# Performance work log

Measured on AMD Instinct MI355X. Metric: run time of the kernel, lower is better.

## Reference

```python
import jax, jax.numpy as jnp
import numpy as np

B, NQ, C = 2, 10000, 256
M, L, K = 8, 3, 4
D = C // M
LEVEL_SHAPES = [(100, 100), (50, 50), (25, 25)]


def setup_inputs() -> dict:
    key = jax.random.key(0)
    ks = jax.random.split(key, 16)
    inp = {
        "query": jax.random.normal(ks[0], (B, NQ, C), jnp.float32),
        "reference_points": jax.random.uniform(ks[1], (B, NQ, 2), jnp.float32),
        "value0": jax.random.normal(ks[2], (B, C) + LEVEL_SHAPES[0], jnp.float32),
        "value1": jax.random.normal(ks[3], (B, C) + LEVEL_SHAPES[1], jnp.float32),
        "value2": jax.random.normal(ks[4], (B, C) + LEVEL_SHAPES[2], jnp.float32),
        "Wv": jax.random.normal(ks[5], (C, C), jnp.float32) * 0.02,
        "bv": jnp.zeros((C,), jnp.float32),
        "Ws": jax.random.normal(ks[6], (M * L * K * 2, C), jnp.float32) * 0.05,
        "bs": jax.random.normal(ks[7], (M * L * K * 2,), jnp.float32),
        "Wa": jax.random.normal(ks[8], (M * L * K, C), jnp.float32) * 0.02,
        "ba": jnp.zeros((M * L * K,), jnp.float32),
        "Wo": jax.random.normal(ks[9], (C, C), jnp.float32) * 0.02,
        "bo": jnp.zeros((C,), jnp.float32),
    }
    return inp


def _bilinear_sample(vflat, px, py, H, W):
    """grid_sample bilinear, align_corners=False, padding_mode='zeros'.
    vflat: (B, M, H*W, D); px, py: (B, M, Q, K) pixel coords. -> (B, M, Q, K, D)
    """
    b, m, q, k = px.shape
    x0 = jnp.floor(px)
    y0 = jnp.floor(py)
    wx1 = px - x0  # frac weights (grad 1 w.r.t. px, matching grid_sample)
    wy1 = py - y0
    wx0 = 1.0 - wx1
    wy0 = 1.0 - wy1

    def gather(xi, yi):
        valid = ((xi >= 0) & (xi <= W - 1) & (yi >= 0) & (yi <= H - 1)).astype(vflat.dtype)
        xc = jnp.clip(xi, 0, W - 1).astype(jnp.int32)
        yc = jnp.clip(yi, 0, H - 1).astype(jnp.int32)
        idx = (yc * W + xc).reshape(b, m, q * k)
        g = jnp.take_along_axis(vflat, idx[..., None], axis=2)  # (B,M,QK,D)
        return g.reshape(b, m, q, k, -1) * valid[..., None]

    out = (gather(x0, y0) * (wx0 * wy0)[..., None]
           + gather(x0 + 1, y0) * (wx1 * wy0)[..., None]
           + gather(x0, y0 + 1) * (wx0 * wy1)[..., None]
           + gather(x0 + 1, y0 + 1) * (wx1 * wy1)[..., None])
    return out


def reference(query, reference_points, value0, value1, value2,
              Wv, bv, Ws, bs, Wa, ba, Wo, bo):
    bsz, nq, c = query.shape
    dt = query.dtype
    # sampling offsets and attention weights
    off = (query @ Ws.T + bs).reshape(bsz, nq, M, L, K, 2)
    attn = jax.nn.softmax((query @ Wa.T + ba).reshape(bsz, nq, M, L * K), axis=-1)
    attn = attn.reshape(bsz, nq, M, L, K)

    out = jnp.zeros((bsz, nq, M, D), dt)
    for li, v in enumerate([value0, value1, value2]):
        H, W = v.shape[2], v.shape[3]
        # conv1x1 value projection -> per-head maps (B, M, H*W, D)
        proj = jnp.einsum('bchw,oc->bohw', v, Wv) + bv[None, :, None, None]
        vflat = proj.reshape(bsz, M, D, H * W).transpose(0, 1, 3, 2)
        norm = jnp.asarray([W, H], dt)
        loc = reference_points[:, :, None, None, :] + off[:, :, :, li, :, :] / norm  # (B,Q,M,K,2)
        # grid = loc*2-1; pixel = (grid+1)*size/2 - 0.5 = loc*size - 0.5
        px = (loc[..., 0] * W - 0.5).transpose(0, 2, 1, 3)  # (B,M,Q,K)
        py = (loc[..., 1] * H - 0.5).transpose(0, 2, 1, 3)
        sampled = _bilinear_sample(vflat, px, py, H, W)  # (B,M,Q,K,D)
        out = out + jnp.einsum('bmqkd,bqmk->bqmd', sampled, attn[:, :, :, li, :])

    out = out.reshape(bsz, nq, c)
    return out @ Wo.T + bo
```

## Files before the change

### kernel.cpp

```cpp
#include <hip/hip_runtime.h>
#include <cstddef>

#define B_ 2
#define NQ_ 10000
#define C_ 256
#define M_ 8
#define L_ 3
#define K_ 4
#define D_ 32
#define P_ 13125

typedef unsigned short u16;
typedef __attribute__((ext_vector_type(8))) short short8;
typedef __attribute__((ext_vector_type(4))) float f32x4;

static __device__ __forceinline__ u16 f2bf(float f) {
    union { float f; unsigned u; } x; x.f = f;
    unsigned r = x.u + 0x7fffu + ((x.u >> 16) & 1u);
    return (u16)(r >> 16);
}
static __device__ __forceinline__ short8 cvt8(const float4& a, const float4& b) {
    short8 r;
    r[0] = (short)f2bf(a.x); r[1] = (short)f2bf(a.y);
    r[2] = (short)f2bf(a.z); r[3] = (short)f2bf(a.w);
    r[4] = (short)f2bf(b.x); r[5] = (short)f2bf(b.y);
    r[6] = (short)f2bf(b.z); r[7] = (short)f2bf(b.w);
    return r;
}

__global__ __launch_bounds__(256) void cvt_f32_bf16(
    const float* __restrict__ in, u16* __restrict__ out, int n8)
{
    const int i = blockIdx.x * 256 + threadIdx.x;
    if (i >= n8) return;
    const float4 a = *reinterpret_cast<const float4*>(in + (size_t)i * 8);
    const float4 b = *reinterpret_cast<const float4*>(in + (size_t)i * 8 + 4);
    *reinterpret_cast<short8*>(out + (size_t)i * 8) = cvt8(a, b);
}

__global__ __launch_bounds__(256) void cvt_weights(
    const float* __restrict__ Wv, const float* __restrict__ Ws,
    const float* __restrict__ Wa, const float* __restrict__ Wo,
    u16* __restrict__ wb)
{
    const int i = blockIdx.x * 256 + threadIdx.x;
    if (i >= 25600) return;
    const int g = i * 8;
    const float* src;
    if (g < 65536)       src = Wv + g;
    else if (g < 114688) src = Ws + (g - 65536);
    else if (g < 139264) src = Wa + (g - 114688);
    else                 src = Wo + (g - 139264);
    const float4 a = *reinterpret_cast<const float4*>(src);
    const float4 b = *reinterpret_cast<const float4*>(src + 4);
    *reinterpret_cast<short8*>(wb + g) = cvt8(a, b);
}

__global__ __launch_bounds__(256) void transpose_value(
    const float* __restrict__ v0, const float* __restrict__ v1,
    const float* __restrict__ v2, u16* __restrict__ Vt)
{
    constexpr int HWs[3]  = {10000, 2500, 625};
    constexpr int offs[3] = {0, 10000, 12500};

    const int z   = blockIdx.z;
    const int b   = z / 3;
    const int lvl = z % 3;
    const int HW  = HWs[lvl];
    const int p0  = blockIdx.x * 64;
    if (p0 >= HW) return;
    const int c0  = blockIdx.y * 64;

    const float* V = (lvl == 0 ? v0 : (lvl == 1 ? v1 : v2)) + (size_t)b * 256 * HW;

    __shared__ u16 tile[64][66];
    const int t  = threadIdx.x;
    const int pl = t & 63;
    const int cb = t >> 6;

    #pragma unroll
    for (int i = 0; i < 16; ++i) {
        int c = cb + i * 4;
        float vv = 0.f;
        if (p0 + pl < HW)
            vv = V[(size_t)(c0 + c) * HW + p0 + pl];
        tile[pl][c] = f2bf(vv);
    }
    __syncthreads();

    const int cl = t & 63;
    const int pb = t >> 6;
    #pragma unroll
    for (int i = 0; i < 16; ++i) {
        int p = pb + i * 4;
        if (p0 + p < HW)
            Vt[((size_t)b * P_ + offs[lvl] + p0 + p) * 256 + c0 + cl] = tile[p][cl];
    }
}

__global__ __launch_bounds__(512) void gemm_fused(
    const u16* __restrict__ Vt, const u16* __restrict__ qbf,
    const u16* __restrict__ Wvb, const float* __restrict__ bv,
    const u16* __restrict__ Wsb, const float* __restrict__ bs,
    const u16* __restrict__ Wab, const float* __restrict__ ba,
    u16* __restrict__ proj, float* __restrict__ S)
{
    __shared__ u16 Bs[64 * 264];

    const bool jobS = (blockIdx.x >= 416);
    const int  bid  = jobS ? (blockIdx.x - 416) : blockIdx.x;

    const int npanel    = jobS ? 5 : 4;
    const int nRowTiles = jobS ? 79 : 103;
    const int rows      = jobS ? (B_ * NQ_) : (B_ * P_);
    const int N1        = jobS ? 192 : 256;
    const int Ntot      = jobS ? 288 : 256;
    const u16* Aimg     = jobS ? qbf : Vt;
    const u16* B1b      = jobS ? Wsb : Wvb;
    const u16* B2b      = jobS ? Wab : Wvb;
    const float* bias1  = jobS ? bs : bv;
    const float* bias2  = jobS ? ba : bv;

    const int rlo  = bid & 7;
    const int tmp  = bid >> 3;
    const int panel = tmp % npanel;
    const int rowTile = (tmp / npanel) * 8 + rlo;
    if (rowTile >= nRowTiles) return;

    const int t  = threadIdx.x;
    const int w  = t >> 6;
    const int l  = t & 63;
    const int row0 = rowTile * 256 + w * 32;
    const int o0   = panel * 64;
    const int lr = l & 15;
    const int kb = (l >> 4) * 8;

    const int ra0 = min(row0 + lr,      rows - 1);
    const int ra1 = min(row0 + 16 + lr, rows - 1);
    const u16* Ap0 = Aimg + (size_t)ra0 * 256 + kb;
    const u16* Ap1 = Aimg + (size_t)ra1 * 256 + kb;

    short8 A0[4], A1[4];
    #pragma unroll
    for (int i = 0; i < 4; ++i) {
        A0[i] = *reinterpret_cast<const short8*>(Ap0 + i * 32);
        A1[i] = *reinterpret_cast<const short8*>(Ap1 + i * 32);
    }

    #pragma unroll
    for (int i = 0; i < 4; ++i) {
        int idx = i * 512 + t;
        int col = idx >> 5;
        int kc  = (idx & 31) * 8;
        int colg = min(o0 + col, Ntot - 1);
        const u16* Br = ((colg < N1) ? B1b + (size_t)colg * 256
                                     : B2b + (size_t)(colg - N1) * 256) + kc;
        *reinterpret_cast<short8*>(&Bs[col * 264 + kc]) =
            *reinterpret_cast<const short8*>(Br);
    }

    __syncthreads();

    short8 A0b[4], A1b[4];
    #pragma unroll
    for (int i = 0; i < 4; ++i) {
        A0b[i] = *reinterpret_cast<const short8*>(Ap0 + 128 + i * 32);
        A1b[i] = *reinterpret_cast<const short8*>(Ap1 + 128 + i * 32);
    }

    f32x4 acc[2][4] = {};
    #pragma unroll
    for (int i = 0; i < 8; ++i) {
        const int k0 = i * 32;
        short8 a0 = (i < 4) ? A0[i] : A0b[i - 4];
        short8 a1 = (i < 4) ? A1[i] : A1b[i - 4];
        short8 b0 = *reinterpret_cast<const short8*>(&Bs[(0 * 16 + lr) * 264 + kb + k0]);
        short8 b1 = *reinterpret_cast<const short8*>(&Bs[(1 * 16 + lr) * 264 + kb + k0]);
        short8 b2 = *reinterpret_cast<const short8*>(&Bs[(2 * 16 + lr) * 264 + kb + k0]);
        short8 b3 = *reinterpret_cast<const short8*>(&Bs[(3 * 16 + lr) * 264 + kb + k0]);
        acc[0][0] = __builtin_amdgcn_mfma_f32_16x16x32_bf16(a0, b0, acc[0][0], 0, 0, 0);
        acc[0][1] = __builtin_amdgcn_mfma_f32_16x16x32_bf16(a0, b1, acc[0][1], 0, 0, 0);
        acc[0][2] = __builtin_amdgcn_mfma_f32_16x16x32_bf16(a0, b2, acc[0][2], 0, 0, 0);
        acc[0][3] = __builtin_amdgcn_mfma_f32_16x16x32_bf16(a0, b3, acc[0][3], 0, 0, 0);
        acc[1][0] = __builtin_amdgcn_mfma_f32_16x16x32_bf16(a1, b0, acc[1][0], 0, 0, 0);
        acc[1][1] = __builtin_amdgcn_mfma_f32_16x16x32_bf16(a1, b1, acc[1][1], 0, 0, 0);
        acc[1][2] = __builtin_amdgcn_mfma_f32_16x16x32_bf16(a1, b2, acc[1][2], 0, 0, 0);
        acc[1][3] = __builtin_amdgcn_mfma_f32_16x16x32_bf16(a1, b3, acc[1][3], 0, 0, 0);
    }

    const int orow = (l >> 4) * 4;
    #pragma unroll
    for (int ct = 0; ct < 4; ++ct) {
        const int col = o0 + ct * 16 + lr;
        if (col >= Ntot) continue;
        const float bsv = (col < N1) ? bias1[col] : bias2[col - N1];
        #pragma unroll
        for (int rt = 0; rt < 2; ++rt) {
            #pragma unroll
            for (int r = 0; r < 4; ++r) {
                const int row = row0 + rt * 16 + orow + r;
                if (row < rows) {
                    float val = acc[rt][ct][r] + bsv;
                    if (jobS)
                        S[(size_t)row * 288 + col] = val;
                    else
                        proj[(size_t)row * 256 + col] = f2bf(val);
                }
            }
        }
    }
}

__global__ __launch_bounds__(512) void gemm_out(
    const u16* __restrict__ Av, int rows, int nRowTiles, int npanel,
    const u16* __restrict__ Bb, const float* __restrict__ bias, int Ntot,
    float* __restrict__ Cout)
{
    __shared__ u16 Bs[64 * 264];

    const int bid  = blockIdx.x;
    const int rlo  = bid & 7;
    const int tmp  = bid >> 3;
    const int panel = tmp % npanel;
    const int rowTile = (tmp / npanel) * 8 + rlo;
    if (rowTile >= nRowTiles) return;

    const int t  = threadIdx.x;
    const int w  = t >> 6;
    const int l  = t & 63;
    const int row0 = rowTile * 256 + w * 32;
    const int o0   = panel * 64;
    const int lr = l & 15;
    const int kb = (l >> 4) * 8;

    const int ra0 = min(row0 + lr,      rows - 1);
    const int ra1 = min(row0 + 16 + lr, rows - 1);
    const u16* Ap0 = Av + (size_t)ra0 * 256 + kb;
    const u16* Ap1 = Av + (size_t)ra1 * 256 + kb;

    short8 A0[4], A1[4];
    #pragma unroll
    for (int i = 0; i < 4; ++i) {
        A0[i] = *reinterpret_cast<const short8*>(Ap0 + i * 32);
        A1[i] = *reinterpret_cast<const short8*>(Ap1 + i * 32);
    }

    #pragma unroll
    for (int i = 0; i < 4; ++i) {
        int idx = i * 512 + t;
        int col = idx >> 5;
        int kc  = (idx & 31) * 8;
        int colg = min(o0 + col, Ntot - 1);
        *reinterpret_cast<short8*>(&Bs[col * 264 + kc]) =
            *reinterpret_cast<const short8*>(Bb + (size_t)colg * 256 + kc);
    }

    __syncthreads();

    short8 A0b[4], A1b[4];
    #pragma unroll
    for (int i = 0; i < 4; ++i) {
        A0b[i] = *reinterpret_cast<const short8*>(Ap0 + 128 + i * 32);
        A1b[i] = *reinterpret_cast<const short8*>(Ap1 + 128 + i * 32);
    }

    f32x4 acc[2][4] = {};
    #pragma unroll
    for (int i = 0; i < 8; ++i) {
        const int k0 = i * 32;
        short8 a0 = (i < 4) ? A0[i] : A0b[i - 4];
        short8 a1 = (i < 4) ? A1[i] : A1b[i - 4];
        short8 b0 = *reinterpret_cast<const short8*>(&Bs[(0 * 16 + lr) * 264 + kb + k0]);
        short8 b1 = *reinterpret_cast<const short8*>(&Bs[(1 * 16 + lr) * 264 + kb + k0]);
        short8 b2 = *reinterpret_cast<const short8*>(&Bs[(2 * 16 + lr) * 264 + kb + k0]);
        short8 b3 = *reinterpret_cast<const short8*>(&Bs[(3 * 16 + lr) * 264 + kb + k0]);
        acc[0][0] = __builtin_amdgcn_mfma_f32_16x16x32_bf16(a0, b0, acc[0][0], 0, 0, 0);
        acc[0][1] = __builtin_amdgcn_mfma_f32_16x16x32_bf16(a0, b1, acc[0][1], 0, 0, 0);
        acc[0][2] = __builtin_amdgcn_mfma_f32_16x16x32_bf16(a0, b2, acc[0][2], 0, 0, 0);
        acc[0][3] = __builtin_amdgcn_mfma_f32_16x16x32_bf16(a0, b3, acc[0][3], 0, 0, 0);
        acc[1][0] = __builtin_amdgcn_mfma_f32_16x16x32_bf16(a1, b0, acc[1][0], 0, 0, 0);
        acc[1][1] = __builtin_amdgcn_mfma_f32_16x16x32_bf16(a1, b1, acc[1][1], 0, 0, 0);
        acc[1][2] = __builtin_amdgcn_mfma_f32_16x16x32_bf16(a1, b2, acc[1][2], 0, 0, 0);
        acc[1][3] = __builtin_amdgcn_mfma_f32_16x16x32_bf16(a1, b3, acc[1][3], 0, 0, 0);
    }

    const int orow = (l >> 4) * 4;
    #pragma unroll
    for (int ct = 0; ct < 4; ++ct) {
        const int col = o0 + ct * 16 + lr;
        if (col >= Ntot) continue;
        const float bsv = bias[col];
        #pragma unroll
        for (int rt = 0; rt < 2; ++rt) {
            #pragma unroll
            for (int r = 0; r < 4; ++r) {
                const int row = row0 + rt * 16 + orow + r;
                if (row < rows)
                    Cout[(size_t)row * Ntot + col] = acc[rt][ct][r] + bsv;
            }
        }
    }
}

__global__ __launch_bounds__(256) void sample_kernel(
    const float* __restrict__ S,
    const float* __restrict__ refp,
    const u16* __restrict__ proj,
    u16* __restrict__ out2)
{
    constexpr int Wd[3]   = {100, 50, 25};
    constexpr int offs[3] = {0, 10000, 12500};

    __shared__ int   midx[192][4];
    __shared__ float mw[192][4];

    const int t = threadIdx.x;

    if (t < 192) {
        const int q  = t / 96;
        const int tq = t % 96;
        const int tm = tq / 12;
        const int tj = tq % 12;
        const int bq = blockIdx.x * 2 + q;
        const float* Sq = S + (size_t)bq * 288;

        float lg[12], mx = -1e30f;
        #pragma unroll
        for (int jj = 0; jj < 12; ++jj) {
            lg[jj] = Sq[192 + tm * 12 + jj];
            mx = fmaxf(mx, lg[jj]);
        }
        float sum = 0.f;
        #pragma unroll
        for (int jj = 0; jj < 12; ++jj) sum += __expf(lg[jj] - mx);
        const float attn = __expf(lg[tj] - mx) / sum;

        const int l  = tj >> 2;
        const int Wl = Wd[l];
        const float refx = refp[(size_t)bq * 2 + 0];
        const float refy = refp[(size_t)bq * 2 + 1];
        const float ox = Sq[(tm * 12 + tj) * 2 + 0];
        const float oy = Sq[(tm * 12 + tj) * 2 + 1];
        const float px = refx * (float)Wl + ox - 0.5f;
        const float py = refy * (float)Wl + oy - 0.5f;
        const float x0f = floorf(px), y0f = floorf(py);
        const float wx1 = px - x0f, wy1 = py - y0f;
        const float wx0 = 1.f - wx1, wy0 = 1.f - wy1;
        const int x0 = (int)x0f, y0 = (int)y0f;
        const int x1 = x0 + 1, y1 = y0 + 1;
        const bool vx0 = (unsigned)x0 < (unsigned)Wl;
        const bool vx1 = (unsigned)x1 < (unsigned)Wl;
        const bool vy0 = (unsigned)y0 < (unsigned)Wl;
        const bool vy1 = (unsigned)y1 < (unsigned)Wl;
        const int chb  = tm * 32;
        const int base = offs[l];
        midx[t][0] = (vx0 && vy0) ? ((base + y0 * Wl + x0) * 256 + chb) : 0;
        midx[t][1] = (vx1 && vy0) ? ((base + y0 * Wl + x1) * 256 + chb) : 0;
        midx[t][2] = (vx0 && vy1) ? ((base + y1 * Wl + x0) * 256 + chb) : 0;
        midx[t][3] = (vx1 && vy1) ? ((base + y1 * Wl + x1) * 256 + chb) : 0;
        mw[t][0] = (vx0 && vy0) ? attn * wx0 * wy0 : 0.f;
        mw[t][1] = (vx1 && vy0) ? attn * wx1 * wy0 : 0.f;
        mw[t][2] = (vx0 && vy1) ? attn * wx0 * wy1 : 0.f;
        mw[t][3] = (vx1 && vy1) ? attn * wx1 * wy1 : 0.f;
    }
    __syncthreads();

    const int qi  = t >> 7;
    const int tt  = t & 127;
    const int mh  = tt >> 4;
    const int d16 = tt & 15;
    const int bq2 = blockIdx.x * 2 + qi;
    const int b   = bq2 / NQ_;
    const u16* projb = proj + (size_t)b * P_ * 256 + 2 * d16;

    float acc0 = 0.f, acc1 = 0.f;

    #pragma unroll
    for (int j = 0; j < 12; ++j) {
        const int mj = qi * 96 + mh * 12 + j;
        const int4   o  = *reinterpret_cast<const int4*>(midx[mj]);
        const float4 ww = *reinterpret_cast<const float4*>(mw[mj]);
        const unsigned u00 = *reinterpret_cast<const unsigned*>(projb + o.x);
        const unsigned u10 = *reinterpret_cast<const unsigned*>(projb + o.y);
        const unsigned u01 = *reinterpret_cast<const unsigned*>(projb + o.z);
        const unsigned u11 = *reinterpret_cast<const unsigned*>(projb + o.w);
        union { unsigned u; float f; } c0, c1;
        c0.u = u00 << 16;          c1.u = u00 & 0xffff0000u;
        acc0 = fmaf(ww.x, c0.f, acc0); acc1 = fmaf(ww.x, c1.f, acc1);
        c0.u = u10 << 16;          c1.u = u10 & 0xffff0000u;
        acc0 = fmaf(ww.y, c0.f, acc0); acc1 = fmaf(ww.y, c1.f, acc1);
        c0.u = u01 << 16;          c1.u = u01 & 0xffff0000u;
        acc0 = fmaf(ww.z, c0.f, acc0); acc1 = fmaf(ww.z, c1.f, acc1);
        c0.u = u11 << 16;          c1.u = u11 & 0xffff0000u;
        acc0 = fmaf(ww.w, c0.f, acc0); acc1 = fmaf(ww.w, c1.f, acc1);
    }

    const unsigned packed = (unsigned)f2bf(acc0) | ((unsigned)f2bf(acc1) << 16);
    *reinterpret_cast<unsigned*>(out2 + (size_t)bq2 * 256 + mh * 32 + 2 * d16) = packed;
}

extern "C" void kernel_launch(void* const* d_in, const int* in_sizes, int n_in,
                              void* d_out, int out_size, void* d_ws, size_t ws_size,
                              hipStream_t stream)
{
    const float* query = (const float*)d_in[0];
    const float* refp  = (const float*)d_in[1];
    const float* v0    = (const float*)d_in[2];
    const float* v1    = (const float*)d_in[3];
    const float* v2    = (const float*)d_in[4];
    const float* Wv    = (const float*)d_in[5];
    const float* bv    = (const float*)d_in[6];
    const float* Ws    = (const float*)d_in[7];
    const float* bs    = (const float*)d_in[8];
    const float* Wa    = (const float*)d_in[9];
    const float* ba    = (const float*)d_in[10];
    const float* Wo    = (const float*)d_in[11];
    const float* bo    = (const float*)d_in[12];
    float* out = (float*)d_out;

    char* wsb = (char*)d_ws;
    u16*   proj  = (u16*)wsb;    wsb += (size_t)B_ * P_ * 256 * 2;
    float* S     = (float*)wsb;  wsb += (size_t)B_ * NQ_ * 288 * 4;
    u16*   Vt    = (u16*)wsb;    wsb += (size_t)B_ * P_ * 256 * 2;
    u16*   out2  = (u16*)wsb;    wsb += (size_t)B_ * NQ_ * 256 * 2;
    u16*   qbf   = (u16*)wsb;    wsb += (size_t)B_ * NQ_ * 256 * 2;
    u16*   wb    = (u16*)wsb;    wsb += (size_t)204800 * 2;
    u16* Wvb = wb;
    u16* Wsb = wb + 65536;
    u16* Wab = wb + 114688;
    u16* Wob = wb + 139264;

    cvt_weights<<<dim3(100), dim3(256), 0, stream>>>(Wv, Ws, Wa, Wo, wb);

    cvt_f32_bf16<<<dim3(2500), dim3(256), 0, stream>>>(query, qbf, 640000);

    transpose_value<<<dim3(157, 4, 6), dim3(256), 0, stream>>>(v0, v1, v2, Vt);

    gemm_fused<<<dim3(816), dim3(512), 0, stream>>>(
        Vt, qbf, Wvb, bv, Wsb, bs, Wab, ba, proj, S);

    sample_kernel<<<dim3(NQ_), dim3(256), 0, stream>>>(S, refp, proj, out2);

    gemm_out<<<dim3(320), dim3(512), 0, stream>>>(
        out2, B_ * NQ_, 79, 4, Wob, bo, 256, out);
}
```

Measured before the change: 202.4 us.

## Merge prep kernels into one launch and widen sampling to four queries per block

The three preprocessing kernels (value transpose, weight conversion, query conversion) are merged into a single launch whose branch is chosen by block index, removing two launch gaps. The sampling kernel now handles four queries per block instead of two. Each query-head softmax is computed once into shared memory rather than redundantly by twelve threads, and each thread gathers four bf16 channels per corner with 8-byte loads. The trade-offs are more shared memory per block and fewer threads covering each query's channels.

```diff
diff --git a/kernel.cpp b/kernel.cpp
--- a/kernel.cpp
+++ b/kernel.cpp
@@ -28,73 +28,70 @@
     return r;
 }
 
-__global__ __launch_bounds__(256) void cvt_f32_bf16(
-    const float* __restrict__ in, u16* __restrict__ out, int n8)
-{
-    const int i = blockIdx.x * 256 + threadIdx.x;
-    if (i >= n8) return;
-    const float4 a = *reinterpret_cast<const float4*>(in + (size_t)i * 8);
-    const float4 b = *reinterpret_cast<const float4*>(in + (size_t)i * 8 + 4);
-    *reinterpret_cast<short8*>(out + (size_t)i * 8) = cvt8(a, b);
-}
-
-__global__ __launch_bounds__(256) void cvt_weights(
+__global__ __launch_bounds__(256) void prep(
+    const float* __restrict__ v0, const float* __restrict__ v1,
+    const float* __restrict__ v2, u16* __restrict__ Vt,
     const float* __restrict__ Wv, const float* __restrict__ Ws,
     const float* __restrict__ Wa, const float* __restrict__ Wo,
-    u16* __restrict__ wb)
+    u16* __restrict__ wb,
+    const float* __restrict__ query, u16* __restrict__ qbf)
 {
-    const int i = blockIdx.x * 256 + threadIdx.x;
-    if (i >= 25600) return;
-    const int g = i * 8;
-    const float* src;
-    if (g < 65536)       src = Wv + g;
-    else if (g < 114688) src = Ws + (g - 65536);
-    else if (g < 139264) src = Wa + (g - 114688);
-    else                 src = Wo + (g - 139264);
-    const float4 a = *reinterpret_cast<const float4*>(src);
-    const float4 b = *reinterpret_cast<const float4*>(src + 4);
-    *reinterpret_cast<short8*>(wb + g) = cvt8(a, b);
-}
-
-__global__ __launch_bounds__(256) void transpose_value(
-    const float* __restrict__ v0, const float* __restrict__ v1,
-    const float* __restrict__ v2, u16* __restrict__ Vt)
-{
-    constexpr int HWs[3]  = {10000, 2500, 625};
-    constexpr int offs[3] = {0, 10000, 12500};
-
-    const int z   = blockIdx.z;
-    const int b   = z / 3;
-    const int lvl = z % 3;
-    const int HW  = HWs[lvl];
-    const int p0  = blockIdx.x * 64;
-    if (p0 >= HW) return;
-    const int c0  = blockIdx.y * 64;
-
-    const float* V = (lvl == 0 ? v0 : (lvl == 1 ? v1 : v2)) + (size_t)b * 256 * HW;
-
     __shared__ u16 tile[64][66];
-    const int t  = threadIdx.x;
-    const int pl = t & 63;
-    const int cb = t >> 6;
-
-    #pragma unroll
-    for (int i = 0; i < 16; ++i) {
-        int c = cb + i * 4;
-        float vv = 0.f;
-        if (p0 + pl < HW)
-            vv = V[(size_t)(c0 + c) * HW + p0 + pl];
-        tile[pl][c] = f2bf(vv);
-    }
-    __syncthreads();
-
-    const int cl = t & 63;
-    const int pb = t >> 6;
-    #pragma unroll
-    for (int i = 0; i < 16; ++i) {
-        int p = pb + i * 4;
-        if (p0 + p < HW)
-            Vt[((size_t)b * P_ + offs[lvl] + p0 + p) * 256 + c0 + cl] = tile[p][cl];
+    const int bid = blockIdx.x;
+    const int t   = threadIdx.x;
+
+    if (bid < 3768) {
+        constexpr int HWs[3]  = {10000, 2500, 625};
+        constexpr int offs[3] = {0, 10000, 12500};
+        const int x = bid % 157;
+        const int y = (bid / 157) % 4;
+        const int z = bid / 628;
+        const int b   = z / 3;
+        const int lvl = z % 3;
+        const int HW  = HWs[lvl];
+        const int p0  = x * 64;
+        if (p0 >= HW) return;
+        const int c0  = y * 64;
+
+        const float* V = (lvl == 0 ? v0 : (lvl == 1 ? v1 : v2)) + (size_t)b * 256 * HW;
+
+        const int pl = t & 63;
+        const int cb = t >> 6;
+        #pragma unroll
+        for (int i = 0; i < 16; ++i) {
+            int c = cb + i * 4;
+            float vv = 0.f;
+            if (p0 + pl < HW)
+                vv = V[(size_t)(c0 + c) * HW + p0 + pl];
+            tile[pl][c] = f2bf(vv);
+        }
+        __syncthreads();
+
+        const int cl = t & 63;
+        const int pb = t >> 6;
+        #pragma unroll
+        for (int i = 0; i < 16; ++i) {
+            int p = pb + i * 4;
+            if (p0 + p < HW)
+                Vt[((size_t)b * P_ + offs[lvl] + p0 + p) * 256 + c0 + cl] = tile[p][cl];
+        }
+    } else if (bid < 3868) {
+        const int i = (bid - 3768) * 256 + t;
+        if (i >= 25600) return;
+        const int g = i * 8;
+        const float* src;
+        if (g < 65536)       src = Wv + g;
+        else if (g < 114688) src = Ws + (g - 65536);
+        else if (g < 139264) src = Wa + (g - 114688);
+        else                 src = Wo + (g - 139264);
+        const float4 a = *reinterpret_cast<const float4*>(src);
+        const float4 b = *reinterpret_cast<const float4*>(src + 4);
+        *reinterpret_cast<short8*>(wb + g) = cvt8(a, b);
+    } else {
+        const int i = (bid - 3868) * 256 + t;
+        const float4 a = *reinterpret_cast<const float4*>(query + (size_t)i * 8);
+        const float4 b = *reinterpret_cast<const float4*>(query + (size_t)i * 8 + 4);
+        *reinterpret_cast<short8*>(qbf + (size_t)i * 8) = cvt8(a, b);
     }
 }
 
@@ -311,29 +308,37 @@
     constexpr int Wd[3]   = {100, 50, 25};
     constexpr int offs[3] = {0, 10000, 12500};
 
-    __shared__ int   midx[192][4];
-    __shared__ float mw[192][4];
+    __shared__ float attnS[32][12];
+    __shared__ int   midx[384][4];
+    __shared__ float mw[384][4];
 
     const int t = threadIdx.x;
 
-    if (t < 192) {
-        const int q  = t / 96;
-        const int tq = t % 96;
+    if (t < 32) {
+        const int q = t >> 3;
+        const int m = t & 7;
+        const int bq = blockIdx.x * 4 + q;
+        const float* Sq = S + (size_t)bq * 288 + 192 + m * 12;
+        float lg[12], mx = -1e30f;
+        #pragma unroll
+        for (int j = 0; j < 12; ++j) { lg[j] = Sq[j]; mx = fmaxf(mx, lg[j]); }
+        float sum = 0.f;
+        #pragma unroll
+        for (int j = 0; j < 12; ++j) { lg[j] = __expf(lg[j] - mx); sum += lg[j]; }
+        const float rs = 1.0f / sum;
+        #pragma unroll
+        for (int j = 0; j < 12; ++j) attnS[t][j] = lg[j] * rs;
+    }
+    __syncthreads();
+
+    for (int job = t; job < 384; job += 256) {
+        const int q  = job / 96;
+        const int tq = job % 96;
         const int tm = tq / 12;
         const int tj = tq % 12;
-        const int bq = blockIdx.x * 2 + q;
+        const int bq = blockIdx.x * 4 + q;
         const float* Sq = S + (size_t)bq * 288;
-
-        float lg[12], mx = -1e30f;
-        #pragma unroll
-        for (int jj = 0; jj < 12; ++jj) {
-            lg[jj] = Sq[192 + tm * 12 + jj];
-            mx = fmaxf(mx, lg[jj]);
-        }
-        float sum = 0.f;
-        #pragma unroll
-        for (int jj = 0; jj < 12; ++jj) sum += __expf(lg[jj] - mx);
-        const float attn = __expf(lg[tj] - mx) / sum;
+        const float attn = attnS[q * 8 + tm][tj];
 
         const int l  = tj >> 2;
         const int Wl = Wd[l];
@@ -354,49 +359,59 @@
         const bool vy1 = (unsigned)y1 < (unsigned)Wl;
         const int chb  = tm * 32;
         const int base = offs[l];
-        midx[t][0] = (vx0 && vy0) ? ((base + y0 * Wl + x0) * 256 + chb) : 0;
-        midx[t][1] = (vx1 && vy0) ? ((base + y0 * Wl + x1) * 256 + chb) : 0;
-        midx[t][2] = (vx0 && vy1) ? ((base + y1 * Wl + x0) * 256 + chb) : 0;
-        midx[t][3] = (vx1 && vy1) ? ((base + y1 * Wl + x1) * 256 + chb) : 0;
-        mw[t][0] = (vx0 && vy0) ? attn * wx0 * wy0 : 0.f;
-        mw[t][1] = (vx1 && vy0) ? attn * wx1 * wy0 : 0.f;
-        mw[t][2] = (vx0 && vy1) ? attn * wx0 * wy1 : 0.f;
-        mw[t][3] = (vx1 && vy1) ? attn * wx1 * wy1 : 0.f;
+        midx[job][0] = (vx0 && vy0) ? ((base + y0 * Wl + x0) * 256 + chb) : 0;
+        midx[job][1] = (vx1 && vy0) ? ((base + y0 * Wl + x1) * 256 + chb) : 0;
+        midx[job][2] = (vx0 && vy1) ? ((base + y1 * Wl + x0) * 256 + chb) : 0;
+        midx[job][3] = (vx1 && vy1) ? ((base + y1 * Wl + x1) * 256 + chb) : 0;
+        mw[job][0] = (vx0 && vy0) ? attn * wx0 * wy0 : 0.f;
+        mw[job][1] = (vx1 && vy0) ? attn * wx1 * wy0 : 0.f;
+        mw[job][2] = (vx0 && vy1) ? attn * wx0 * wy1 : 0.f;
+        mw[job][3] = (vx1 && vy1) ? attn * wx1 * wy1 : 0.f;
     }
     __syncthreads();
 
-    const int qi  = t >> 7;
-    const int tt  = t & 127;
-    const int mh  = tt >> 4;
-    const int d16 = tt & 15;
-    const int bq2 = blockIdx.x * 2 + qi;
+    const int qi  = t >> 6;
+    const int tt  = t & 63;
+    const int mh  = tt >> 3;
+    const int d8  = tt & 7;
+    const int bq2 = blockIdx.x * 4 + qi;
     const int b   = bq2 / NQ_;
-    const u16* projb = proj + (size_t)b * P_ * 256 + 2 * d16;
-
-    float acc0 = 0.f, acc1 = 0.f;
+    const u16* projb = proj + (size_t)b * P_ * 256 + 4 * d8;
+    const int base_mj = qi * 96 + mh * 12;
+
+    float acc0 = 0.f, acc1 = 0.f, acc2 = 0.f, acc3 = 0.f;
 
     #pragma unroll
     for (int j = 0; j < 12; ++j) {
-        const int mj = qi * 96 + mh * 12 + j;
-        const int4   o  = *reinterpret_cast<const int4*>(midx[mj]);
-        const float4 ww = *reinterpret_cast<const float4*>(mw[mj]);
-        const unsigned u00 = *reinterpret_cast<const unsigned*>(projb + o.x);
-        const unsigned u10 = *reinterpret_cast<const unsigned*>(projb + o.y);
-        const unsigned u01 = *reinterpret_cast<const unsigned*>(projb + o.z);
-        const unsigned u11 = *reinterpret_cast<const unsigned*>(projb + o.w);
-        union { unsigned u; float f; } c0, c1;
-        c0.u = u00 << 16;          c1.u = u00 & 0xffff0000u;
-        acc0 = fmaf(ww.x, c0.f, acc0); acc1 = fmaf(ww.x, c1.f, acc1);
-        c0.u = u10 << 16;          c1.u = u10 & 0xffff0000u;
-        acc0 = fmaf(ww.y, c0.f, acc0); acc1 = fmaf(ww.y, c1.f, acc1);
-        c0.u = u01 << 16;          c1.u = u01 & 0xffff0000u;
-        acc0 = fmaf(ww.z, c0.f, acc0); acc1 = fmaf(ww.z, c1.f, acc1);
-        c0.u = u11 << 16;          c1.u = u11 & 0xffff0000u;
-        acc0 = fmaf(ww.w, c0.f, acc0); acc1 = fmaf(ww.w, c1.f, acc1);
-    }
-
-    const unsigned packed = (unsigned)f2bf(acc0) | ((unsigned)f2bf(acc1) << 16);
-    *reinterpret_cast<unsigned*>(out2 + (size_t)bq2 * 256 + mh * 32 + 2 * d16) = packed;
+        const int4   o  = *reinterpret_cast<const int4*>(midx[base_mj + j]);
+        const float4 ww = *reinterpret_cast<const float4*>(mw[base_mj + j]);
+        const uint2 v00 = *reinterpret_cast<const uint2*>(projb + o.x);
+        const uint2 v10 = *reinterpret_cast<const uint2*>(projb + o.y);
+        const uint2 v01 = *reinterpret_cast<const uint2*>(projb + o.z);
+        const uint2 v11 = *reinterpret_cast<const uint2*>(projb + o.w);
+        union { unsigned u; float f; } e0, e1, e2, e3;
+        e0.u = v00.x << 16; e1.u = v00.x & 0xffff0000u;
+        e2.u = v00.y << 16; e3.u = v00.y & 0xffff0000u;
+        acc0 = fmaf(ww.x, e0.f, acc0); acc1 = fmaf(ww.x, e1.f, acc1);
+        acc2 = fmaf(ww.x, e2.f, acc2); acc3 = fmaf(ww.x, e3.f, acc3);
+        e0.u = v10.x << 16; e1.u = v10.x & 0xffff0000u;
+        e2.u = v10.y << 16; e3.u = v10.y & 0xffff0000u;
+        acc0 = fmaf(ww.y, e0.f, acc0); acc1 = fmaf(ww.y, e1.f, acc1);
+        acc2 = fmaf(ww.y, e2.f, acc2); acc3 = fmaf(ww.y, e3.f, acc3);
+        e0.u = v01.x << 16; e1.u = v01.x & 0xffff0000u;
+        e2.u = v01.y << 16; e3.u = v01.y & 0xffff0000u;
+        acc0 = fmaf(ww.z, e0.f, acc0); acc1 = fmaf(ww.z, e1.f, acc1);
+        acc2 = fmaf(ww.z, e2.f, acc2); acc3 = fmaf(ww.z, e3.f, acc3);
+        e0.u = v11.x << 16; e1.u = v11.x & 0xffff0000u;
+        e2.u = v11.y << 16; e3.u = v11.y & 0xffff0000u;
+        acc0 = fmaf(ww.w, e0.f, acc0); acc1 = fmaf(ww.w, e1.f, acc1);
+        acc2 = fmaf(ww.w, e2.f, acc2); acc3 = fmaf(ww.w, e3.f, acc3);
+    }
+
+    uint2 st;
+    st.x = (unsigned)f2bf(acc0) | ((unsigned)f2bf(acc1) << 16);
+    st.y = (unsigned)f2bf(acc2) | ((unsigned)f2bf(acc3) << 16);
+    *reinterpret_cast<uint2*>(out2 + (size_t)bq2 * 256 + mh * 32 + d8 * 4) = st;
 }
 
 extern "C" void kernel_launch(void* const* d_in, const int* in_sizes, int n_in,
@@ -430,16 +445,13 @@
     u16* Wab = wb + 114688;
     u16* Wob = wb + 139264;
 
-    cvt_weights<<<dim3(100), dim3(256), 0, stream>>>(Wv, Ws, Wa, Wo, wb);
-
-    cvt_f32_bf16<<<dim3(2500), dim3(256), 0, stream>>>(query, qbf, 640000);
-
-    transpose_value<<<dim3(157, 4, 6), dim3(256), 0, stream>>>(v0, v1, v2, Vt);
+    prep<<<dim3(6368), dim3(256), 0, stream>>>(
+        v0, v1, v2, Vt, Wv, Ws, Wa, Wo, wb, query, qbf);
 
     gemm_fused<<<dim3(816), dim3(512), 0, stream>>>(
         Vt, qbf, Wvb, bv, Wsb, bs, Wab, ba, proj, S);
 
-    sample_kernel<<<dim3(NQ_), dim3(256), 0, stream>>>(S, refp, proj, out2);
+    sample_kernel<<<dim3(5000), dim3(256), 0, stream>>>(S, refp, proj, out2);
 
     gemm_out<<<dim3(320), dim3(512), 0, stream>>>(
         out2, B_ * NQ_, 79, 4, Wob, bo, 256, out);
```

New measurement: 202.7 us. Within noise of the previous version (+0.1%).
